# Performance work log

Hardware: AMD Instinct MI355X
Metric: run time of the kernel (lower is better)

Reference implementation:

```python
import jax, jax.numpy as jnp
import numpy as np


def setup_inputs() -> dict:
    key = jax.random.key(0)
    k1, k2, k3 = jax.random.split(key, 3)
    B, IN, H, OUT = 2048, 4096, 4096, 1024
    x = jax.random.normal(k1, (B, IN), dtype=jnp.float32)
    fc1_weight = jax.random.randint(k2, (H, IN), 0, 2).astype(jnp.int32)
    fc2_weight = jax.random.randint(k3, (OUT, H), 0, 2).astype(jnp.int32)
    return {"x": x, "fc1_weight": fc1_weight, "fc2_weight": fc2_weight, "threshold": 2048}


def _binary_popcount_matmul(a, w):
    # a: (B, K) in {0,1}, w: (N, K) in {0,1}
    # matches = sum_k 1 - (a XOR w) = a@w.T + (1-a)@(1-w).T  (identical math,
    # avoids materializing the (B, N, K) XNOR tensor the naive code builds)
    return jnp.einsum('bk,nk->bn', a, w) + jnp.einsum('bk,nk->bn', 1 - a, 1 - w)


def reference(x, fc1_weight, fc2_weight, threshold):
    xb = (x.reshape(x.shape[0], -1) >= 0).astype(jnp.int32)   # binarize input
    pc1 = _binary_popcount_matmul(xb, fc1_weight)              # (B, H) popcounts
    act1 = (pc1 >= threshold).astype(jnp.int32)                # threshold activation
    pc2 = _binary_popcount_matmul(act1, fc2_weight)            # (B, OUT) popcounts
    return pc2
```

## Files before the change

### kernel.cpp

```cpp
#include <hip/hip_runtime.h>
#include <stdint.h>

typedef int v4i  __attribute__((ext_vector_type(4)));
typedef int v16i __attribute__((ext_vector_type(16)));

__device__ __forceinline__ void gload_lds16(const void* g, void* l) {
    __builtin_amdgcn_global_load_lds(
        (const __attribute__((address_space(1))) void*)g,
        (__attribute__((address_space(3))) void*)l, 16, 0, 0);
}

template<typename T, bool ISFLOAT>
__global__ __launch_bounds__(256)
void pack_frag(const T* __restrict__ in, int8_t* __restrict__ F, int K) {
    __shared__ int8_t lbuf[32 * 1040];
    const int t  = threadIdx.x;
    const int db = blockIdx.y;
    const int c0 = blockIdx.x * 1024;

    #pragma unroll 4
    for (int r = 0; r < 32; ++r) {
        uint32_t b;
        if constexpr (ISFLOAT) {
            const float4 v = *(const float4*)(in + (size_t)(db * 32 + r) * K + c0 + t * 4);
            b =  (v.x >= 0.0f ? 0x01u : 0xFFu)
              | ((v.y >= 0.0f ? 0x01u : 0xFFu) << 8)
              | ((v.z >= 0.0f ? 0x01u : 0xFFu) << 16)
              | ((v.w >= 0.0f ? 0x01u : 0xFFu) << 24);
        } else {
            const int4 v = *(const int4*)(in + (size_t)(db * 32 + r) * K + c0 + t * 4);
            b =  (v.x ? 0x01u : 0xFFu)
              | ((v.y ? 0x01u : 0xFFu) << 8)
              | ((v.z ? 0x01u : 0xFFu) << 16)
              | ((v.w ? 0x01u : 0xFFu) << 24);
        }
        *(uint32_t*)(lbuf + r * 1040 + t * 4) = b;
    }
    __syncthreads();

    const int s  = t >> 3;
    const int l0 = (t & 7) * 8;
    const int KC = K >> 5;
    int8_t* dst = F + ((size_t)db * KC + blockIdx.x * 32 + s) * 1024 + l0 * 16;
    #pragma unroll
    for (int li = 0; li < 8; ++li) {
        int l = l0 + li;
        uint4 v = *(const uint4*)(lbuf + (l & 31) * 1040 + s * 32 + (l >> 5) * 16);
        *(uint4*)(dst + li * 16) = v;
    }
}

template<int WN, bool PACK_OUT>
__global__ __launch_bounds__(256, 1)
void bnn_mfma(const int8_t* __restrict__ Af,
              const int8_t* __restrict__ Bf,
              const int* __restrict__ thr_ptr,
              int8_t* __restrict__ actf,
              int* __restrict__ out, int Nout)
{
    constexpr int KC     = 128;
    constexpr int NKT    = 64;
    constexpr int NBB    = 2 * WN;
    constexpr int ASLOTS = 512;
    constexpr int BSLOTS = 128 * NBB;
    constexpr int SLOTS  = ASLOTS + BSLOTS;
    constexpr int NLD    = SLOTS / 256;
    constexpr uint32_t BUFSZ = (uint32_t)SLOTS * 16;

    __shared__ int8_t lds[3][SLOTS * 16];

    const int tid  = threadIdx.x;
    const int lane = tid & 63;
    const int wv   = tid >> 6;
    const int wr   = wv >> 1, wc = wv & 1;

    const int g   = blockIdx.x;
    const int idx = g >> 3;
    const int bn  = (g & 7) * 2 + (idx >> 4);
    const int bm  = idx & 15;

    const int8_t* gsrc[NLD];
    uint32_t ldoff[NLD];
    #pragma unroll
    for (int i = 0; i < NLD; ++i) {
        int sbase = wv * 64 + 256 * i;
        ldoff[i] = (uint32_t)sbase * 16;
        const int8_t* base;
        if (sbase < ASLOTS) {
            int R = sbase >> 7, C = (sbase >> 6) & 1;
            base = Af + ((size_t)(bm * 4 + R) * KC + C) * 1024;
        } else {
            int s = sbase - ASLOTS;
            int R = s >> 7, C = (s >> 6) & 1;
            base = Bf + ((size_t)(bn * NBB + R) * KC + C) * 1024;
        }
        gsrc[i] = base + lane * 16;
    }

    auto stage = [&](int buf) {
        #pragma unroll
        for (int i = 0; i < NLD; ++i) {
            gload_lds16(gsrc[i], (int8_t*)lds + (uint32_t)buf * BUFSZ + ldoff[i]);
            gsrc[i] += 2048;
        }
    };

    v16i acc[2][WN];
    #pragma unroll
    for (int i = 0; i < 2; ++i)
        #pragma unroll
        for (int j = 0; j < WN; ++j) acc[i][j] = {};

    stage(0);
    stage(1);

    int cur = 0, nxt = 2;
    #pragma unroll 1
    for (int kt = 0; kt < NKT; ++kt) {
        if (kt < NKT - 1) {
            if constexpr (NLD == 6) asm volatile("s_waitcnt vmcnt(6)" ::: "memory");
            else                    asm volatile("s_waitcnt vmcnt(3)" ::: "memory");
        } else {
            asm volatile("s_waitcnt vmcnt(0)" ::: "memory");
        }
        __builtin_amdgcn_sched_barrier(0);
        __builtin_amdgcn_s_barrier();
        __builtin_amdgcn_sched_barrier(0);

        if (kt < NKT - 2) {
            stage(nxt);
            nxt = (nxt == 2) ? 0 : nxt + 1;
        }

        const int8_t* Al = lds[cur];
        const int8_t* Bl = lds[cur] + ASLOTS * 16;
        #pragma unroll
        for (int kc = 0; kc < 2; ++kc) {
            v4i af[2], bf[WN];
            #pragma unroll
            for (int i = 0; i < 2; ++i)
                af[i] = *(const v4i*)(Al + (((wr * 2 + i) * 2 + kc) * 64 + lane) * 16);
            #pragma unroll
            for (int j = 0; j < WN; ++j)
                bf[j] = *(const v4i*)(Bl + (((wc * WN + j) * 2 + kc) * 64 + lane) * 16);
            #pragma unroll
            for (int i = 0; i < 2; ++i)
                #pragma unroll
                for (int j = 0; j < WN; ++j)
                    acc[i][j] = __builtin_amdgcn_mfma_i32_32x32x32_i8(af[i], bf[j], acc[i][j], 0, 0, 0);
        }
        cur = (cur == 2) ? 0 : cur + 1;
    }

    if constexpr (PACK_OUT) {
        __syncthreads();
        const int thr = *thr_ptr;
        int8_t* bits = (int8_t*)lds;
        #pragma unroll
        for (int i = 0; i < 2; ++i)
            #pragma unroll
            for (int j = 0; j < WN; ++j) {
                int dimb = wr * 64 + i * 32 + 4 * (lane >> 5);
                int gcl  = wc * (32 * WN) + j * 32 + (lane & 31);
                #pragma unroll
                for (int reg = 0; reg < 16; ++reg) {
                    int dl = dimb + (reg & 3) + 8 * (reg >> 2);
                    int match = (4096 + acc[i][j][reg]) >> 1;
                    bits[dl * 272 + gcl] = (match >= thr) ? (int8_t)1 : (int8_t)-1;
                }
            }
        __syncthreads();
        const int s    = tid >> 3;
        const int dblk = s >> 3, kcl = s & 7;
        const int l0   = (tid & 7) * 8;
        int8_t* dst = actf + ((size_t)(bm * 4 + dblk) * KC + bn * 8 + kcl) * 1024 + l0 * 16;
        #pragma unroll
        for (int li = 0; li < 8; ++li) {
            int l = l0 + li;
            uint4 v = *(const uint4*)(bits + (dblk * 32 + (l & 31)) * 272
                                           + kcl * 32 + (l >> 5) * 16);
            *(uint4*)(dst + li * 16) = v;
        }
    } else {
        #pragma unroll
        for (int i = 0; i < 2; ++i)
            #pragma unroll
            for (int j = 0; j < WN; ++j) {
                int gc = bn * (64 * WN) + wc * (32 * WN) + j * 32 + (lane & 31);
                #pragma unroll
                for (int reg = 0; reg < 16; ++reg) {
                    int gr = bm * 128 + wr * 64 + i * 32
                           + (reg & 3) + 8 * (reg >> 2) + 4 * (lane >> 5);
                    out[(size_t)gr * Nout + gc] = (4096 + acc[i][j][reg]) >> 1;
                }
            }
    }
}

extern "C" void kernel_launch(void* const* d_in, const int* in_sizes, int n_in,
                              void* d_out, int out_size, void* d_ws, size_t ws_size,
                              hipStream_t stream) {
    const float* x   = (const float*)d_in[0];
    const int*   w1  = (const int*)d_in[1];
    const int*   w2  = (const int*)d_in[2];
    const int*   thr = (const int*)d_in[3];
    int* out = (int*)d_out;

    const int B = 2048, IN = 4096, H = 4096, OUT = 1024;
    uint8_t* ws = (uint8_t*)d_ws;

    int8_t* Af  = (int8_t*)(ws);
    int8_t* W1f = (int8_t*)(ws + ((size_t)8  << 20));
    int8_t* W2f = (int8_t*)(ws + ((size_t)24 << 20));
    int8_t* Act = (int8_t*)(ws + ((size_t)28 << 20));

    pack_frag<float, true ><<<dim3(IN / 1024, B   / 32), 256, 0, stream>>>(x,  Af,  IN);
    pack_frag<int,   false><<<dim3(IN / 1024, H   / 32), 256, 0, stream>>>(w1, W1f, IN);
    pack_frag<int,   false><<<dim3(H  / 1024, OUT / 32), 256, 0, stream>>>(w2, W2f, H);

    bnn_mfma<4, true ><<<256, 256, 0, stream>>>(Af,  W1f, thr, Act, nullptr, 0);
    bnn_mfma<1, false><<<256, 256, 0, stream>>>(Act, W2f, nullptr, nullptr, out, OUT);
}
```

Before: 96.33 us.

## Split layer-1 GEMM into 8-wave kernel with phased loads and MFMA priority

Result: faster. 92.15 us (-4.3%).

```diff
diff --git a/kernel.cpp b/kernel.cpp
--- a/kernel.cpp
+++ b/kernel.cpp
@@ -11,52 +11,186 @@
 }
 
 template<typename T, bool ISFLOAT>
-__global__ __launch_bounds__(256)
+__global__ __launch_bounds__(512)
 void pack_frag(const T* __restrict__ in, int8_t* __restrict__ F, int K) {
     __shared__ int8_t lbuf[32 * 1040];
     const int t  = threadIdx.x;
     const int db = blockIdx.y;
-    const int c0 = blockIdx.x * 1024;
-
-    #pragma unroll 4
-    for (int r = 0; r < 32; ++r) {
+    const int c0 = blockIdx.x << 10;
+
+    #pragma unroll
+    for (int p = 0; p < 16; ++p) {
+        int idx = p * 512 + t;
+        int row = idx >> 8, c4 = idx & 255;
         uint32_t b;
         if constexpr (ISFLOAT) {
-            const float4 v = *(const float4*)(in + (size_t)(db * 32 + r) * K + c0 + t * 4);
+            const float4 v = *(const float4*)(in + (size_t)(db * 32 + row) * K + c0 + c4 * 4);
             b =  (v.x >= 0.0f ? 0x01u : 0xFFu)
               | ((v.y >= 0.0f ? 0x01u : 0xFFu) << 8)
               | ((v.z >= 0.0f ? 0x01u : 0xFFu) << 16)
               | ((v.w >= 0.0f ? 0x01u : 0xFFu) << 24);
         } else {
-            const int4 v = *(const int4*)(in + (size_t)(db * 32 + r) * K + c0 + t * 4);
+            const int4 v = *(const int4*)(in + (size_t)(db * 32 + row) * K + c0 + c4 * 4);
             b =  (v.x ? 0x01u : 0xFFu)
               | ((v.y ? 0x01u : 0xFFu) << 8)
               | ((v.z ? 0x01u : 0xFFu) << 16)
               | ((v.w ? 0x01u : 0xFFu) << 24);
         }
-        *(uint32_t*)(lbuf + r * 1040 + t * 4) = b;
+        *(uint32_t*)(lbuf + row * 1040 + c4 * 4) = b;
     }
     __syncthreads();
 
-    const int s  = t >> 3;
-    const int l0 = (t & 7) * 8;
+    const int s  = t >> 4;
+    const int l0 = (t & 15) * 4;
     const int KC = K >> 5;
-    int8_t* dst = F + ((size_t)db * KC + blockIdx.x * 32 + s) * 1024 + l0 * 16;
-    #pragma unroll
-    for (int li = 0; li < 8; ++li) {
+    int8_t* dst = F + ((size_t)db * KC + blockIdx.x * 32 + s) * 1024;
+    #pragma unroll
+    for (int li = 0; li < 4; ++li) {
         int l = l0 + li;
         uint4 v = *(const uint4*)(lbuf + (l & 31) * 1040 + s * 32 + (l >> 5) * 16);
-        *(uint4*)(dst + li * 16) = v;
-    }
-}
-
-template<int WN, bool PACK_OUT>
+        *(uint4*)(dst + l * 16) = v;
+    }
+}
+
+__global__ __launch_bounds__(512, 2)
+void bnn_l1_8w(const int8_t* __restrict__ Af,
+               const int8_t* __restrict__ Bf,
+               const int* __restrict__ thr_ptr,
+               int8_t* __restrict__ actf)
+{
+    constexpr int KC  = 128;
+    constexpr int NKT = 64;
+    constexpr uint32_t BUFSZ = 24576;
+
+    __shared__ int8_t lds[3 * 24576];
+
+    const int tid  = threadIdx.x;
+    const int lane = tid & 63;
+    const int wv   = tid >> 6;
+    const int wr   = wv >> 2, wc = wv & 3;
+
+    const int g   = blockIdx.x;
+    const int idx = g >> 3;
+    const int bn  = (g & 7) * 2 + (idx >> 4);
+    const int bm  = idx & 15;
+
+    const int8_t* gsrc[3];
+    uint32_t loff[3];
+    #pragma unroll
+    for (int c = 0; c < 3; ++c) {
+        int s = c * 512 + tid;
+        if (s < 512) {
+            int R = s >> 7, kk = (s >> 6) & 1, ln = s & 63;
+            gsrc[c] = Af + ((size_t)(bm * 4 + R) * KC + kk) * 1024 + ln * 16;
+            loff[c] = (uint32_t)s * 16;
+        } else {
+            int s2 = s - 512;
+            int Cb = s2 >> 7, kk = (s2 >> 6) & 1, ln = s2 & 63;
+            gsrc[c] = Bf + ((size_t)(bn * 8 + Cb) * KC + kk) * 1024 + ln * 16;
+            loff[c] = 8192u + (uint32_t)s2 * 16;
+        }
+    }
+
+    auto issue = [&](int c, uint32_t bufo) {
+        gload_lds16(gsrc[c], lds + bufo + loff[c]);
+        gsrc[c] += 2048;
+    };
+
+    v16i acc[2][2];
+    #pragma unroll
+    for (int i = 0; i < 2; ++i)
+        #pragma unroll
+        for (int j = 0; j < 2; ++j) acc[i][j] = {};
+
+    issue(0, 0); issue(1, 0); issue(2, 0);
+    issue(0, BUFSZ); issue(1, BUFSZ); issue(2, BUFSZ);
+
+    uint32_t bo = 0;
+    #pragma unroll 1
+    for (int kt = 0; kt < NKT; ++kt) {
+        if (kt + 1 < NKT) asm volatile("s_waitcnt vmcnt(3)" ::: "memory");
+        else              asm volatile("s_waitcnt vmcnt(0)" ::: "memory");
+        __builtin_amdgcn_sched_barrier(0);
+        __builtin_amdgcn_s_barrier();
+        __builtin_amdgcn_sched_barrier(0);
+
+        const uint32_t sbo = (bo >= BUFSZ) ? (bo - BUFSZ) : (2 * BUFSZ);
+        const int8_t* Ab = lds + bo + wr * 4096 + lane * 16;
+        const int8_t* Bb = lds + bo + 8192 + wc * 4096 + lane * 16;
+
+        {
+            v4i af0 = *(const v4i*)(Ab + 0);
+            v4i af1 = *(const v4i*)(Ab + 2048);
+            v4i bf0 = *(const v4i*)(Bb + 0);
+            v4i bf1 = *(const v4i*)(Bb + 2048);
+            if (kt + 2 < NKT) { issue(0, sbo); issue(1, sbo); }
+            __builtin_amdgcn_s_barrier();
+            asm volatile("s_waitcnt lgkmcnt(0)" ::: "memory");
+            __builtin_amdgcn_sched_barrier(0);
+            __builtin_amdgcn_s_setprio(1);
+            acc[0][0] = __builtin_amdgcn_mfma_i32_32x32x32_i8(af0, bf0, acc[0][0], 0, 0, 0);
+            acc[0][1] = __builtin_amdgcn_mfma_i32_32x32x32_i8(af0, bf1, acc[0][1], 0, 0, 0);
+            acc[1][0] = __builtin_amdgcn_mfma_i32_32x32x32_i8(af1, bf0, acc[1][0], 0, 0, 0);
+            acc[1][1] = __builtin_amdgcn_mfma_i32_32x32x32_i8(af1, bf1, acc[1][1], 0, 0, 0);
+            __builtin_amdgcn_s_setprio(0);
+            __builtin_amdgcn_sched_barrier(0);
+            __builtin_amdgcn_s_barrier();
+        }
+        {
+            v4i af0 = *(const v4i*)(Ab + 1024);
+            v4i af1 = *(const v4i*)(Ab + 3072);
+            v4i bf0 = *(const v4i*)(Bb + 1024);
+            v4i bf1 = *(const v4i*)(Bb + 3072);
+            if (kt + 2 < NKT) issue(2, sbo);
+            __builtin_amdgcn_s_barrier();
+            asm volatile("s_waitcnt lgkmcnt(0)" ::: "memory");
+            __builtin_amdgcn_sched_barrier(0);
+            __builtin_amdgcn_s_setprio(1);
+            acc[0][0] = __builtin_amdgcn_mfma_i32_32x32x32_i8(af0, bf0, acc[0][0], 0, 0, 0);
+            acc[0][1] = __builtin_amdgcn_mfma_i32_32x32x32_i8(af0, bf1, acc[0][1], 0, 0, 0);
+            acc[1][0] = __builtin_amdgcn_mfma_i32_32x32x32_i8(af1, bf0, acc[1][0], 0, 0, 0);
+            acc[1][1] = __builtin_amdgcn_mfma_i32_32x32x32_i8(af1, bf1, acc[1][1], 0, 0, 0);
+            __builtin_amdgcn_s_setprio(0);
+            __builtin_amdgcn_sched_barrier(0);
+        }
+        bo = (bo == 2 * BUFSZ) ? 0u : bo + BUFSZ;
+    }
+
+    __syncthreads();
+    const int thr = *thr_ptr;
+    int8_t* bits = lds;
+    #pragma unroll
+    for (int i = 0; i < 2; ++i)
+        #pragma unroll
+        for (int j = 0; j < 2; ++j) {
+            int dimb = wr * 64 + i * 32 + 4 * (lane >> 5);
+            int gcl  = wc * 64 + j * 32 + (lane & 31);
+            #pragma unroll
+            for (int reg = 0; reg < 16; ++reg) {
+                int dl = dimb + (reg & 3) + 8 * (reg >> 2);
+                int match = (4096 + acc[i][j][reg]) >> 1;
+                bits[dl * 272 + gcl] = (match >= thr) ? (int8_t)1 : (int8_t)-1;
+            }
+        }
+    __syncthreads();
+    const int s    = tid >> 4;
+    const int dblk = s >> 3, kcl = s & 7;
+    const int l0   = (tid & 15) * 4;
+    int8_t* dst = actf + ((size_t)(bm * 4 + dblk) * KC + bn * 8 + kcl) * 1024;
+    #pragma unroll
+    for (int li = 0; li < 4; ++li) {
+        int l = l0 + li;
+        uint4 v = *(const uint4*)(bits + (dblk * 32 + (l & 31)) * 272
+                                       + kcl * 32 + (l >> 5) * 16);
+        *(uint4*)(dst + l * 16) = v;
+    }
+}
+
+template<int WN>
 __global__ __launch_bounds__(256, 1)
-void bnn_mfma(const int8_t* __restrict__ Af,
-              const int8_t* __restrict__ Bf,
-              const int* __restrict__ thr_ptr,
-              int8_t* __restrict__ actf,
-              int* __restrict__ out, int Nout)
+void bnn_mfma2(const int8_t* __restrict__ Af,
+               const int8_t* __restrict__ Bf,
+               int* __restrict__ out, int Nout)
 {
     constexpr int KC     = 128;
     constexpr int NKT    = 64;
@@ -117,12 +251,8 @@
     int cur = 0, nxt = 2;
     #pragma unroll 1
     for (int kt = 0; kt < NKT; ++kt) {
-        if (kt < NKT - 1) {
-            if constexpr (NLD == 6) asm volatile("s_waitcnt vmcnt(6)" ::: "memory");
-            else                    asm volatile("s_waitcnt vmcnt(3)" ::: "memory");
-        } else {
-            asm volatile("s_waitcnt vmcnt(0)" ::: "memory");
-        }
+        if (kt < NKT - 1) asm volatile("s_waitcnt vmcnt(3)" ::: "memory");
+        else              asm volatile("s_waitcnt vmcnt(0)" ::: "memory");
         __builtin_amdgcn_sched_barrier(0);
         __builtin_amdgcn_s_barrier();
         __builtin_amdgcn_sched_barrier(0);
@@ -152,49 +282,18 @@
         cur = (cur == 2) ? 0 : cur + 1;
     }
 
-    if constexpr (PACK_OUT) {
-        __syncthreads();
-        const int thr = *thr_ptr;
-        int8_t* bits = (int8_t*)lds;
-        #pragma unroll
-        for (int i = 0; i < 2; ++i)
-            #pragma unroll
-            for (int j = 0; j < WN; ++j) {
-                int dimb = wr * 64 + i * 32 + 4 * (lane >> 5);
-                int gcl  = wc * (32 * WN) + j * 32 + (lane & 31);
-                #pragma unroll
-                for (int reg = 0; reg < 16; ++reg) {
-                    int dl = dimb + (reg & 3) + 8 * (reg >> 2);
-                    int match = (4096 + acc[i][j][reg]) >> 1;
-                    bits[dl * 272 + gcl] = (match >= thr) ? (int8_t)1 : (int8_t)-1;
-                }
+    #pragma unroll
+    for (int i = 0; i < 2; ++i)
+        #pragma unroll
+        for (int j = 0; j < WN; ++j) {
+            int gc = bn * (64 * WN) + wc * (32 * WN) + j * 32 + (lane & 31);
+            #pragma unroll
+            for (int reg = 0; reg < 16; ++reg) {
+                int gr = bm * 128 + wr * 64 + i * 32
+                       + (reg & 3) + 8 * (reg >> 2) + 4 * (lane >> 5);
+                out[(size_t)gr * Nout + gc] = (4096 + acc[i][j][reg]) >> 1;
             }
-        __syncthreads();
-        const int s    = tid >> 3;
-        const int dblk = s >> 3, kcl = s & 7;
-        const int l0   = (tid & 7) * 8;
-        int8_t* dst = actf + ((size_t)(bm * 4 + dblk) * KC + bn * 8 + kcl) * 1024 + l0 * 16;
-        #pragma unroll
-        for (int li = 0; li < 8; ++li) {
-            int l = l0 + li;
-            uint4 v = *(const uint4*)(bits + (dblk * 32 + (l & 31)) * 272
-                                           + kcl * 32 + (l >> 5) * 16);
-            *(uint4*)(dst + li * 16) = v;
-        }
-    } else {
-        #pragma unroll
-        for (int i = 0; i < 2; ++i)
-            #pragma unroll
-            for (int j = 0; j < WN; ++j) {
-                int gc = bn * (64 * WN) + wc * (32 * WN) + j * 32 + (lane & 31);
-                #pragma unroll
-                for (int reg = 0; reg < 16; ++reg) {
-                    int gr = bm * 128 + wr * 64 + i * 32
-                           + (reg & 3) + 8 * (reg >> 2) + 4 * (lane >> 5);
-                    out[(size_t)gr * Nout + gc] = (4096 + acc[i][j][reg]) >> 1;
-                }
-            }
-    }
+        }
 }
 
 extern "C" void kernel_launch(void* const* d_in, const int* in_sizes, int n_in,
@@ -214,10 +313,10 @@
     int8_t* W2f = (int8_t*)(ws + ((size_t)24 << 20));
     int8_t* Act = (int8_t*)(ws + ((size_t)28 << 20));
 
-    pack_frag<float, true ><<<dim3(IN / 1024, B   / 32), 256, 0, stream>>>(x,  Af,  IN);
-    pack_frag<int,   false><<<dim3(IN / 1024, H   / 32), 256, 0, stream>>>(w1, W1f, IN);
-    pack_frag<int,   false><<<dim3(H  / 1024, OUT / 32), 256, 0, stream>>>(w2, W2f, H);
-
-    bnn_mfma<4, true ><<<256, 256, 0, stream>>>(Af,  W1f, thr, Act, nullptr, 0);
-    bnn_mfma<1, false><<<256, 256, 0, stream>>>(Act, W2f, nullptr, nullptr, out, OUT);
-}
+    pack_frag<float, true ><<<dim3(IN / 1024, B   / 32), 512, 0, stream>>>(x,  Af,  IN);
+    pack_frag<int,   false><<<dim3(IN / 1024, H   / 32), 512, 0, stream>>>(w1, W1f, IN);
+    pack_frag<int,   false><<<dim3(H  / 1024, OUT / 32), 512, 0, stream>>>(w2, W2f, H);
+
+    bnn_l1_8w<<<256, 512, 0, stream>>>(Af, W1f, thr, Act);
+    bnn_mfma2<1><<<256, 256, 0, stream>>>(Act, W2f, out, OUT);
+}
```
